# Kernel tuning notes

Measured on AMD Instinct MI355X. Metric: run time of the kernel, lower is better.

Reference implementation:

```python
import jax, jax.numpy as jnp
import numpy as np

E = 1024          # embed_dim
BS = 8            # number of sequences (bs = pre_lf_indexs.shape[0])
L = 8192          # tokens per sequence
N = BS * L        # packed tokens
CACHE = 16384     # lf cache rows
EPS = 1e-6


def setup_inputs() -> dict:
    key = jax.random.key(0)
    ks = jax.random.split(key, 9)
    inputs = jax.random.normal(ks[0], (N, E), jnp.float32)
    conv1_weight = jax.random.normal(ks[1], (E, E), jnp.float32) * (1.0 / np.sqrt(E))
    conv2_weight = jax.random.normal(ks[2], (E // 2, 2 * E), jnp.float32) * (1.0 / np.sqrt(E // 2))
    conv1_bias = jax.random.normal(ks[3], (E // 2,), jnp.float32) * 0.02
    conv2_bias = jax.random.normal(ks[4], (E,), jnp.float32) * 0.02
    ln_weight = jnp.ones((E,), jnp.float32)
    lf1_caches = jax.random.normal(ks[5], (CACHE, E), jnp.float32)
    lf2_caches = jax.random.normal(ks[6], (CACHE, E // 2), jnp.float32)
    # packed layout: each sequence prefixed by one cache slot -> T = N + BS rows
    offs = jnp.arange(BS, dtype=jnp.int32) * (L + 1)
    input_lf_loc = offs                                             # cache slot per seq
    inputs_loc = (offs[:, None] + 1 + jnp.arange(L, dtype=jnp.int32)[None, :]).reshape(-1)
    outputs_loc = inputs_loc - 1                                     # 2-tap causal pairing
    out_lf_loc = offs + L                                            # last token of each seq
    pre_lf_indexs = jax.random.randint(ks[7], (BS,), 0, CACHE, jnp.int32)
    out_lf_indexs = jax.random.randint(ks[8], (BS,), 0, CACHE, jnp.int32)
    return {
        'inputs': inputs, 'conv1_weight': conv1_weight, 'conv2_weight': conv2_weight,
        'conv1_bias': conv1_bias, 'conv2_bias': conv2_bias, 'ln_weight': ln_weight,
        'lf1_caches': lf1_caches, 'lf2_caches': lf2_caches,
        'pre_lf_indexs': pre_lf_indexs, 'out_lf_indexs': out_lf_indexs,
        'input_lf_loc': input_lf_loc, 'out_lf_loc': out_lf_loc,
        'inputs_loc': inputs_loc, 'outputs_loc': outputs_loc,
    }


def _fused_cat_conv2d(x, cache, W, pre_idx, in_lf_loc, in_loc, out_loc):
    # scatter cache rows + token rows into the padded buffer [N+bs, D]
    T = x.shape[0] + pre_idx.shape[0]
    xt = jnp.zeros((T, x.shape[1]), x.dtype)
    xt = xt.at[in_lf_loc].set(cache[pre_idx])   # gather from lf cache
    xt = xt.at[in_loc].set(x)
    co = xt @ W                                  # [T, 2*Dout]
    h = co.shape[1] // 2
    # shifted 2-tap causal conv: pair row j (prev) with row j+1 (cur)
    ot = co[:-1, :h] + co[1:, h:]                # [T-1, Dout]
    return ot[out_loc]                           # gather back to token order


def reference(inputs, conv1_weight, conv2_weight, conv1_bias, conv2_bias, ln_weight,
              lf1_caches, lf2_caches, pre_lf_indexs, out_lf_indexs,
              input_lf_loc, out_lf_loc, inputs_loc, outputs_loc):
    # (the index_put_ cache writes in the original are side effects for future
    #  steps only; they do not affect this call's output, so they are omitted)
    output1 = _fused_cat_conv2d(inputs, lf1_caches, conv1_weight,
                                pre_lf_indexs, input_lf_loc, inputs_loc, outputs_loc)
    output1 = output1 + conv1_bias               # [N, E/2]
    output2 = _fused_cat_conv2d(output1, lf2_caches, conv2_weight,
                                pre_lf_indexs, input_lf_loc, inputs_loc, outputs_loc)
    output2 = output2 + conv2_bias               # [N, E]
    x = output2 + inputs                         # residual
    var = jnp.mean(x * x, axis=-1, keepdims=True)
    return x * jax.lax.rsqrt(var + EPS) * ln_weight
```

## Files before the change

### kernel.cpp

```cpp
#include <hip/hip_runtime.h>
#include <hip/hip_bf16.h>


#define EDIM 1024
#define HDIM 512
#define LSEQ 8192
#define BSEQ 8
#define SEQR 8193
#define MTOT (BSEQ * SEQR)
#define XROWS 66048

using v8s = __attribute__((ext_vector_type(8))) short;
using v4f = __attribute__((ext_vector_type(4))) float;

__device__ __forceinline__ unsigned short f2b(float f) {
  union { float f; unsigned u; } v; v.f = f;
  unsigned r = v.u + 0x7fffu + ((v.u >> 16) & 1u);
  return (unsigned short)(r >> 16);
}
__device__ __forceinline__ float b2f(unsigned short h) {
  union { unsigned u; float f; } v; v.u = ((unsigned)h) << 16; return v.f;
}
__device__ __forceinline__ void gl_lds16(const void* g, void* l) {
  __builtin_amdgcn_global_load_lds((const __attribute__((address_space(1))) void*)g,
                                   (__attribute__((address_space(3))) void*)l, 16, 0, 0);
}

__device__ __forceinline__ void trns64(const float* __restrict__ src, int src_ld, int src_c0,
                                       unsigned short* __restrict__ dst, int dst_ld, int dst_k0,
                                       int n0, int k0, float (*t)[65], int tx, int ty) {
#pragma unroll
  for (int yy = 0; yy < 64; yy += 4)
    t[yy + ty][tx] = src[(size_t)(k0 + yy + ty) * src_ld + src_c0 + n0 + tx];
  __syncthreads();
#pragma unroll
  for (int yy = 0; yy < 64; yy += 4)
    dst[(size_t)(n0 + yy + ty) * dst_ld + dst_k0 + k0 + tx] = f2b(t[tx][yy + ty]);
}

__global__ __launch_bounds__(256) void prep_all(const float* __restrict__ W1,
                                                const float* __restrict__ W2,
                                                const float* __restrict__ lf2,
                                                const int* __restrict__ preidx,
                                                unsigned short* __restrict__ W1c,
                                                unsigned short* __restrict__ W2c,
                                                unsigned short* __restrict__ c2b) {
  __shared__ float t[64][65];
  const int bk = blockIdx.x;
  const int tid = threadIdx.x;
  if (bk == 512) {
    for (int c = tid; c < HDIM; c += 256)
#pragma unroll
      for (int b = 0; b < BSEQ; ++b)
        c2b[b * HDIM + c] = f2b(lf2[(size_t)preidx[b] * HDIM + c]);
    return;
  }
  const int tx = tid & 63, ty = tid >> 6;
  const int which = bk >> 7, s = bk & 127;
  if (which == 0)       trns64(W1, 1024, 0,    W1c, 2048, 0,    (s & 7) * 64,  (s >> 3) * 64, t, tx, ty);
  else if (which == 1)  trns64(W1, 1024, 512,  W1c, 2048, 1024, (s & 7) * 64,  (s >> 3) * 64, t, tx, ty);
  else if (which == 2)  trns64(W2, 2048, 0,    W2c, 1024, 0,    (s & 15) * 64, (s >> 4) * 64, t, tx, ty);
  else                  trns64(W2, 2048, 1024, W2c, 1024, 512,  (s & 15) * 64, (s >> 4) * 64, t, tx, ty);
}

__global__ __launch_bounds__(256) void cvt_full(const float* __restrict__ inputs,
                                                const float* __restrict__ lf1,
                                                const int* __restrict__ preidx,
                                                unsigned short* __restrict__ Xbf) {
  const int r = blockIdx.x * 4 + (threadIdx.x >> 6);
  const int lane = threadIdx.x & 63;
  unsigned short* dst = Xbf + (size_t)r * EDIM;
  if (r >= MTOT) {
#pragma unroll
    for (int c = lane * 4; c < EDIM; c += 256)
      *(ushort4*)&dst[c] = (ushort4){0, 0, 0, 0};
    return;
  }
  const int b = r / SEQR, rr = r % SEQR;
  const float* src = (rr == 0) ? (lf1 + (size_t)preidx[b] * EDIM)
                               : (inputs + (size_t)(b * LSEQ + rr - 1) * EDIM);
#pragma unroll
  for (int c = lane * 4; c < EDIM; c += 256) {
    const float4 v = *(const float4*)(src + c);
    *(ushort4*)&dst[c] = (ushort4){f2b(v.x), f2b(v.y), f2b(v.z), f2b(v.w)};
  }
}

__global__ __launch_bounds__(512) void fixup_full(const unsigned short* __restrict__ Xbf,
                                                  const unsigned short* __restrict__ W1c,
                                                  const float* __restrict__ b1,
                                                  const unsigned short* __restrict__ c2b,
                                                  unsigned short* __restrict__ A2) {
  const int blk = blockIdx.x;
  const int tid = threadIdx.x;
  if (blk == 7) {
#pragma unroll
    for (int b = 0; b < BSEQ; ++b)
      A2[(size_t)(b * SEQR) * HDIM + tid] = c2b[b * HDIM + tid];
    return;
  }
  const int r = 65536 + blk;
  const unsigned short* a = Xbf + (size_t)r * EDIM;
  const unsigned short* wrow = W1c + (size_t)tid * 2048;
  float s = 0.f;
  for (int k = 0; k < 2048; k += 8) {
    const v8s av = *(const v8s*)&a[k];
    const v8s wv = *(const v8s*)&wrow[k];
#pragma unroll
    for (int j = 0; j < 8; ++j)
      s += b2f((unsigned short)av[j]) * b2f((unsigned short)wv[j]);
  }
  A2[(size_t)(r + 1) * HDIM + tid] = f2b(s + b1[tid]);
}

#define PHASE(p, boA_, off_, ra_)                                                      \
  {                                                                                    \
    v8s af[2][2];                                                                      \
    _Pragma("unroll") for (int m2 = 0; m2 < 2; ++m2)                                   \
    _Pragma("unroll") for (int kx = 0; kx < 2; ++kx)                                   \
      af[m2][kx] = *(const v8s*)&lds[(boA_) +                                          \
          ((2 * (p) + m2) * 32 + wm * 16 + lr + (off_)) * 64 +                         \
          (((kx * 4 + lk) ^ (ra_)) << 3)];                                             \
    __builtin_amdgcn_s_setprio(1);                                                     \
    _Pragma("unroll") for (int m2 = 0; m2 < 2; ++m2)                                   \
    _Pragma("unroll") for (int nc = 0; nc < 4; ++nc)                                   \
    _Pragma("unroll") for (int kx = 0; kx < 2; ++kx)                                   \
      acc[2 * (p) + m2][nc] = __builtin_amdgcn_mfma_f32_16x16x32_bf16(                 \
          af[m2][kx], bf[nc][kx], acc[2 * (p) + m2][nc], 0, 0, 0);                     \
    __builtin_amdgcn_s_setprio(0);                                                     \
  }

#define LOAD_BFR(boB_)                                                                 \
  _Pragma("unroll") for (int nc = 0; nc < 4; ++nc)                                     \
  _Pragma("unroll") for (int kx = 0; kx < 2; ++kx)                                     \
    bf[nc][kx] = *(const v8s*)&lds[(boB_) + (nc * 64 + wn * 16 + lr) * 64 +            \
                                   (((kx * 4 + lk) ^ ra7a) << 3)];

#define STEP4(boA_, off_, ra_)                                                         \
  PHASE(0, boA_, off_, ra_) PHASE(1, boA_, off_, ra_)                                  \
  PHASE(2, boA_, off_, ra_) PHASE(3, boA_, off_, ra_)

template <int K, int NT, bool SHIFTC, bool AMAP>
__global__ __launch_bounds__(512, 2) void gemm_pair(const unsigned short* __restrict__ A,
                                                    const unsigned short* __restrict__ B,
                                                    unsigned short* __restrict__ C,
                                                    const float* __restrict__ bias,
                                                    int q, int r) {
  constexpr int NH = K / 128;
  constexpr int LDA = K / 2;
  constexpr int N = NT * 256;
  constexpr int A0 = 0, A1 = 16512, B_A = 33024, B_B = 49408;
  __shared__ __align__(16) unsigned short lds[65792];

  const int h = blockIdx.x;
  const int xcd = h & 7, idx = h >> 3;
  const int tsw = (xcd < r ? xcd * (q + 1) : r * (q + 1) + (xcd - r) * q) + idx;
  const int mt = tsw / NT, nt = tsw % NT;
  const size_t m0 = (size_t)mt * 256, n0 = (size_t)nt * 256;
  const int tid = threadIdx.x;
  const int w = tid >> 6, lane = tid & 63;
  const int wm = w >> 2, wn = w & 3;
  const int lr = lane & 15, lk = lane >> 4;
  const int ra7a = lr & 7, ra7b = (lr + 1) & 7;
  const int srow = tid >> 3, slot = tid & 7;
  const int gslot = slot ^ (srow & 7);
  const int dAB = srow * 64 + slot * 8;
  const int aBase = (int)m0 + (AMAP ? ((int)m0 >> 13) : 0);

  auto stageApair = [&](int dstE, int i) {
#pragma unroll
    for (int j = 0; j < 4; ++j) {
      const int rr = j * 64 + (tid >> 3);
      gl_lds16(A + (size_t)(aBase + rr) * LDA + i * 64 + ((tid & 7) ^ (rr & 7)) * 8,
               &lds[dstE + rr * 64 + (tid & 7) * 8]);
    }
    if (tid < 8)
      gl_lds16(A + (size_t)(aBase + 256) * LDA + i * 64 + tid * 8,
               &lds[dstE + 256 * 64 + tid * 8]);
  };
  auto stageB = [&](int dstE, int hh, int t) {
    const unsigned short* s = B + (size_t)(n0 + hh * 128 + srow) * K + t * 64 + gslot * 8;
    unsigned short* d = &lds[dstE + hh * 8192 + dAB];
    gl_lds16(s, d);
    gl_lds16(s + (size_t)64 * K, d + 4096);
  };

  v4f acc[8][4];
#pragma unroll
  for (int i = 0; i < 8; ++i)
#pragma unroll
    for (int j = 0; j < 4; ++j) acc[i][j] = (v4f){0.f, 0.f, 0.f, 0.f};

  stageApair(A0, 0);
  stageB(B_A, 0, 0); stageB(B_A, 1, 0);
  asm volatile("s_waitcnt vmcnt(0)" ::: "memory");
  __builtin_amdgcn_s_barrier();

#pragma unroll 1
  for (int i = 0; i < NH - 1; ++i) {
    const int boA = (i & 1) ? A1 : A0;
    const int soA = (i & 1) ? A0 : A1;
    v8s bf[4][2];
    stageB(B_B, 0, i + NH); stageB(B_B, 1, i + NH);
    stageApair(soA, i + 1);
    LOAD_BFR(B_A)
    STEP4(boA, 0, ra7a)
    asm volatile("s_waitcnt vmcnt(4)" ::: "memory");
    __builtin_amdgcn_s_barrier();
    stageB(B_A, 0, i + 1); stageB(B_A, 1, i + 1);
    LOAD_BFR(B_B)
    STEP4(boA, 1, ra7b)
    asm volatile("s_waitcnt vmcnt(0)" ::: "memory");
    __builtin_amdgcn_s_barrier();
  }
  {
    const int boA = ((NH - 1) & 1) ? A1 : A0;
    v8s bf[4][2];
    stageB(B_B, 0, 2 * NH - 1); stageB(B_B, 1, 2 * NH - 1);
    LOAD_BFR(B_A)
    STEP4(boA, 0, ra7a)
    asm volatile("s_waitcnt vmcnt(0)" ::: "memory");
    __builtin_amdgcn_s_barrier();
    LOAD_BFR(B_B)
    STEP4(boA, 1, ra7b)
  }

#pragma unroll
  for (int mr = 0; mr < 8; ++mr)
#pragma unroll
    for (int nc = 0; nc < 4; ++nc) {
      const size_t col = n0 + nc * 64 + wn * 16 + lr;
      float bv = 0.f;
      if constexpr (SHIFTC) bv = bias[col];
#pragma unroll
      for (int g = 0; g < 4; ++g) {
        const size_t row = m0 + mr * 32 + wm * 16 + lk * 4 + g + (SHIFTC ? 1 : 0);
        C[row * N + col] = f2b(acc[mr][nc][g] + bv);
      }
    }
}

__global__ __launch_bounds__(256) void epilogue_full(
    const unsigned short* __restrict__ Zo, const unsigned short* __restrict__ Xbf,
    const float* __restrict__ b2, const float* __restrict__ lnw,
    float* __restrict__ out) {
  const int u = blockIdx.x;
  const size_t rx = (size_t)u + (u >> 13) + 1;
  const int tid = threadIdx.x;
  const int j0 = tid * 4;

  const ushort4 z = *(const ushort4*)&Zo[(size_t)u * EDIM + j0];
  const ushort4 xb = *(const ushort4*)&Xbf[rx * EDIM + j0];
  const float4 bb = *(const float4*)&b2[j0];
  const float4 lw = *(const float4*)&lnw[j0];

  const float x0 = b2f(z.x) + bb.x + b2f(xb.x);
  const float x1 = b2f(z.y) + bb.y + b2f(xb.y);
  const float x2 = b2f(z.z) + bb.z + b2f(xb.z);
  const float x3 = b2f(z.w) + bb.w + b2f(xb.w);

  float ss = x0 * x0 + x1 * x1 + x2 * x2 + x3 * x3;
#pragma unroll
  for (int o = 32; o > 0; o >>= 1) ss += __shfl_xor(ss, o, 64);
  __shared__ float sp[4];
  if ((tid & 63) == 0) sp[tid >> 6] = ss;
  __syncthreads();
  const float tot = sp[0] + sp[1] + sp[2] + sp[3];
  const float scale = rsqrtf(tot * (1.0f / EDIM) + 1e-6f);

  float4 o4;
  o4.x = x0 * scale * lw.x; o4.y = x1 * scale * lw.y;
  o4.z = x2 * scale * lw.z; o4.w = x3 * scale * lw.w;
  *(float4*)&out[(size_t)u * EDIM + j0] = o4;
}

extern "C" void kernel_launch(void* const* d_in, const int* in_sizes, int n_in,
                              void* d_out, int out_size, void* d_ws, size_t ws_size,
                              hipStream_t stream) {
  const float* inputs = (const float*)d_in[0];
  const float* W1 = (const float*)d_in[1];
  const float* W2 = (const float*)d_in[2];
  const float* b1 = (const float*)d_in[3];
  const float* b2 = (const float*)d_in[4];
  const float* lnw = (const float*)d_in[5];
  const float* lf1 = (const float*)d_in[6];
  const float* lf2 = (const float*)d_in[7];
  const int* preidx = (const int*)d_in[8];
  float* out = (float*)d_out;

  char* ws = (char*)d_ws;
  unsigned short* Xbf = (unsigned short*)(ws);
  unsigned short* A2  = (unsigned short*)(ws + 135266304ULL);
  unsigned short* Zo  = (unsigned short*)(ws + 202899456ULL);
  unsigned short* W1c = (unsigned short*)(ws + 337117184ULL);
  unsigned short* W2c = (unsigned short*)(ws + 339214336ULL);
  unsigned short* c2b = (unsigned short*)(ws + 341311488ULL);

  prep_all<<<513, 256, 0, stream>>>(W1, W2, lf2, preidx, W1c, W2c, c2b);
  cvt_full<<<XROWS / 4, 256, 0, stream>>>(inputs, lf1, preidx, Xbf);
  gemm_pair<2048, 2, true, false><<<512, 512, 0, stream>>>(Xbf, W1c, A2, b1, 64, 0);
  fixup_full<<<8, 512, 0, stream>>>(Xbf, W1c, b1, c2b, A2);
  gemm_pair<1024, 4, false, true><<<1024, 512, 0, stream>>>(A2, W2c, Zo, nullptr, 128, 0);
  epilogue_full<<<BSEQ * LSEQ, 256, 0, stream>>>(Zo, Xbf, b2, lnw, out);
}
```

Measured before the change: 471.5 us.

## Switch GEMM inner loop from 16x16x32 to 32x32x16 bf16 MFMA tiles

Replaces the per-wave 16x16x32 MFMA decomposition with 32x32x16 MFMA instructions, reorganizing the A/B fragment LDS reads, the accumulator layout (4x2 v16f instead of 8x4 v4f) and the output row/column mapping. Larger MFMA tiles use fewer LDS fragment loads per flop and fewer instructions, which should cut LDS bandwidth pressure and issue overhead in the GEMM. The trade-off is that each wave now covers a different sub-tile shape, so the XOR swizzle pattern and the epilogue mapping change, with possible LDS bank conflict or register pressure differences.

```diff
diff --git a/kernel.cpp b/kernel.cpp
--- a/kernel.cpp
+++ b/kernel.cpp
@@ -11,7 +11,7 @@
 #define XROWS 66048
 
 using v8s = __attribute__((ext_vector_type(8))) short;
-using v4f = __attribute__((ext_vector_type(4))) float;
+using v16f = __attribute__((ext_vector_type(16))) float;
 
 __device__ __forceinline__ unsigned short f2b(float f) {
   union { float f; unsigned u; } v; v.f = f;
@@ -113,32 +113,33 @@
   A2[(size_t)(r + 1) * HDIM + tid] = f2b(s + b1[tid]);
 }
 
-#define PHASE(p, boA_, off_, ra_)                                                      \
+#define PHASE32(p, boA_, off_)                                                         \
   {                                                                                    \
-    v8s af[2][2];                                                                      \
-    _Pragma("unroll") for (int m2 = 0; m2 < 2; ++m2)                                   \
-    _Pragma("unroll") for (int kx = 0; kx < 2; ++kx)                                   \
-      af[m2][kx] = *(const v8s*)&lds[(boA_) +                                          \
-          ((2 * (p) + m2) * 32 + wm * 16 + lr + (off_)) * 64 +                         \
-          (((kx * 4 + lk) ^ (ra_)) << 3)];                                             \
+    v8s af[4];                                                                         \
+    const int arow = (p) * 64 + wm * 32 + l31 + (off_);                                \
+    const int axr = arow & 7;                                                          \
+    _Pragma("unroll") for (int kk = 0; kk < 4; ++kk)                                   \
+      af[kk] = *(const v8s*)&lds[(boA_) + arow * 64 + (((kk * 2 + lhi) ^ axr) << 3)];  \
     __builtin_amdgcn_s_setprio(1);                                                     \
-    _Pragma("unroll") for (int m2 = 0; m2 < 2; ++m2)                                   \
-    _Pragma("unroll") for (int nc = 0; nc < 4; ++nc)                                   \
-    _Pragma("unroll") for (int kx = 0; kx < 2; ++kx)                                   \
-      acc[2 * (p) + m2][nc] = __builtin_amdgcn_mfma_f32_16x16x32_bf16(                 \
-          af[m2][kx], bf[nc][kx], acc[2 * (p) + m2][nc], 0, 0, 0);                     \
+    _Pragma("unroll") for (int nc = 0; nc < 2; ++nc)                                   \
+    _Pragma("unroll") for (int kk = 0; kk < 4; ++kk)                                   \
+      acc[p][nc] = __builtin_amdgcn_mfma_f32_32x32x16_bf16(                            \
+          af[kk], bfr[nc][kk], acc[p][nc], 0, 0, 0);                                   \
     __builtin_amdgcn_s_setprio(0);                                                     \
   }
 
-#define LOAD_BFR(boB_)                                                                 \
-  _Pragma("unroll") for (int nc = 0; nc < 4; ++nc)                                     \
-  _Pragma("unroll") for (int kx = 0; kx < 2; ++kx)                                     \
-    bf[nc][kx] = *(const v8s*)&lds[(boB_) + (nc * 64 + wn * 16 + lr) * 64 +            \
-                                   (((kx * 4 + lk) ^ ra7a) << 3)];
-
-#define STEP4(boA_, off_, ra_)                                                         \
-  PHASE(0, boA_, off_, ra_) PHASE(1, boA_, off_, ra_)                                  \
-  PHASE(2, boA_, off_, ra_) PHASE(3, boA_, off_, ra_)
+#define LOAD_BFR32(boB_)                                                               \
+  _Pragma("unroll") for (int nc = 0; nc < 2; ++nc) {                                   \
+    const int brow = wn * 64 + nc * 32 + l31;                                          \
+    const int bxr = brow & 7;                                                          \
+    _Pragma("unroll") for (int kk = 0; kk < 4; ++kk)                                   \
+      bfr[nc][kk] = *(const v8s*)&lds[(boB_) + brow * 64 +                             \
+                                      (((kk * 2 + lhi) ^ bxr) << 3)];                  \
+  }
+
+#define STEP32(boA_, off_)                                                             \
+  PHASE32(0, boA_, off_) PHASE32(1, boA_, off_)                                        \
+  PHASE32(2, boA_, off_) PHASE32(3, boA_, off_)
 
 template <int K, int NT, bool SHIFTC, bool AMAP>
 __global__ __launch_bounds__(512, 2) void gemm_pair(const unsigned short* __restrict__ A,
@@ -160,8 +161,7 @@
   const int tid = threadIdx.x;
   const int w = tid >> 6, lane = tid & 63;
   const int wm = w >> 2, wn = w & 3;
-  const int lr = lane & 15, lk = lane >> 4;
-  const int ra7a = lr & 7, ra7b = (lr + 1) & 7;
+  const int l31 = lane & 31, lhi = lane >> 5;
   const int srow = tid >> 3, slot = tid & 7;
   const int gslot = slot ^ (srow & 7);
   const int dAB = srow * 64 + slot * 8;
@@ -185,11 +185,13 @@
     gl_lds16(s + (size_t)64 * K, d + 4096);
   };
 
-  v4f acc[8][4];
-#pragma unroll
-  for (int i = 0; i < 8; ++i)
-#pragma unroll
-    for (int j = 0; j < 4; ++j) acc[i][j] = (v4f){0.f, 0.f, 0.f, 0.f};
+  v16f acc[4][2];
+#pragma unroll
+  for (int i = 0; i < 4; ++i)
+#pragma unroll
+    for (int j = 0; j < 2; ++j)
+#pragma unroll
+      for (int g = 0; g < 16; ++g) acc[i][j][g] = 0.f;
 
   stageApair(A0, 0);
   stageB(B_A, 0, 0); stageB(B_A, 1, 0);
@@ -200,41 +202,42 @@
   for (int i = 0; i < NH - 1; ++i) {
     const int boA = (i & 1) ? A1 : A0;
     const int soA = (i & 1) ? A0 : A1;
-    v8s bf[4][2];
+    v8s bfr[2][4];
     stageB(B_B, 0, i + NH); stageB(B_B, 1, i + NH);
     stageApair(soA, i + 1);
-    LOAD_BFR(B_A)
-    STEP4(boA, 0, ra7a)
+    LOAD_BFR32(B_A)
+    STEP32(boA, 0)
     asm volatile("s_waitcnt vmcnt(4)" ::: "memory");
     __builtin_amdgcn_s_barrier();
     stageB(B_A, 0, i + 1); stageB(B_A, 1, i + 1);
-    LOAD_BFR(B_B)
-    STEP4(boA, 1, ra7b)
+    LOAD_BFR32(B_B)
+    STEP32(boA, 1)
     asm volatile("s_waitcnt vmcnt(0)" ::: "memory");
     __builtin_amdgcn_s_barrier();
   }
   {
     const int boA = ((NH - 1) & 1) ? A1 : A0;
-    v8s bf[4][2];
+    v8s bfr[2][4];
     stageB(B_B, 0, 2 * NH - 1); stageB(B_B, 1, 2 * NH - 1);
-    LOAD_BFR(B_A)
-    STEP4(boA, 0, ra7a)
+    LOAD_BFR32(B_A)
+    STEP32(boA, 0)
     asm volatile("s_waitcnt vmcnt(0)" ::: "memory");
     __builtin_amdgcn_s_barrier();
-    LOAD_BFR(B_B)
-    STEP4(boA, 1, ra7b)
-  }
-
-#pragma unroll
-  for (int mr = 0; mr < 8; ++mr)
-#pragma unroll
-    for (int nc = 0; nc < 4; ++nc) {
-      const size_t col = n0 + nc * 64 + wn * 16 + lr;
+    LOAD_BFR32(B_B)
+    STEP32(boA, 1)
+  }
+
+#pragma unroll
+  for (int mr = 0; mr < 4; ++mr)
+#pragma unroll
+    for (int nc = 0; nc < 2; ++nc) {
+      const size_t col = n0 + wn * 64 + nc * 32 + l31;
       float bv = 0.f;
       if constexpr (SHIFTC) bv = bias[col];
 #pragma unroll
-      for (int g = 0; g < 4; ++g) {
-        const size_t row = m0 + mr * 32 + wm * 16 + lk * 4 + g + (SHIFTC ? 1 : 0);
+      for (int g = 0; g < 16; ++g) {
+        const size_t row = m0 + mr * 64 + wm * 32 + 4 * lhi + (g & 3) + 8 * (g >> 2) +
+                           (SHIFTC ? 1 : 0);
         C[row * N + col] = f2b(acc[mr][nc][g] + bv);
       }
     }
```

Result: slower. 490.7 us (+4.1%).
